# Performance work log

Hardware: AMD Instinct MI355X
Metric: run time of the kernel (lower is better)

Reference implementation:

```python
import jax, jax.numpy as jnp
import numpy as np

B, T, D, U, P, E = 32, 10, 10, 50, 50, 256
EPS_ATTN = 1e-8
EPS_LN = 1e-5


def _layer_norm(x, w, b):
    mu = jnp.mean(x, axis=-1, keepdims=True)
    var = jnp.mean((x - mu) ** 2, axis=-1, keepdims=True)
    return (x - mu) / jnp.sqrt(var + EPS_LN) * w + b


def setup_inputs() -> dict:
    key = jax.random.key(0)
    ks = jax.random.split(key, 8)
    xavier = float(np.sqrt(2.0 / (E + E)))
    return {
        "Q": jax.random.normal(ks[0], (B, T, U, E), dtype=jnp.float32),
        "K": jax.random.normal(ks[1], (B, D, P, E), dtype=jnp.float32),
        "V": jax.random.normal(ks[2], (B, D, P, E), dtype=jnp.float32),
        "attention_mask": jnp.zeros((B, T, D, U, P), dtype=jnp.float32),
        "W1": jax.random.normal(ks[3], (E, E), dtype=jnp.float32) * xavier,
        "b1": jnp.zeros((E,), dtype=jnp.float32),
        "W2": jax.random.normal(ks[4], (E, E), dtype=jnp.float32) * xavier,
        "b2": jnp.zeros((E,), dtype=jnp.float32),
        "ln1_w": jnp.ones((E,), dtype=jnp.float32),
        "ln1_b": jnp.zeros((E,), dtype=jnp.float32),
        "ln2_w": jnp.ones((E,), dtype=jnp.float32),
        "ln2_b": jnp.zeros((E,), dtype=jnp.float32),
    }


def reference(Q, K, V, attention_mask, W1, b1, W2, b2, ln1_w, ln1_b, ln2_w, ln2_b):
    # dk = max(1.0, emb_dim); scale = sqrt(dk) + eps
    scale = jnp.sqrt(jnp.asarray(float(max(1.0, Q.shape[-1])), dtype=Q.dtype)) + EPS_ATTN
    # (B,T,D,U,P) attention logits
    qk = jnp.einsum("btue,bdpe->btdup", Q, K) / scale + attention_mask
    score = jax.nn.softmax(qk, axis=-1)
    v_att = jnp.einsum("btdup,bdpe->btdue", score, V)  # (B,T,D,U,E)
    x = Q[:, :, None, :, :] + v_att  # broadcast over doc dim
    x = _layer_norm(x, ln1_w, ln1_b)
    ffn = jnp.maximum(x @ W1.T + b1, 0.0) @ W2.T + b2
    return _layer_norm(ffn + x, ln2_w, ln2_b)
```

## Files before the change

### kernel.cpp

```cpp
#include <hip/hip_runtime.h>
#include <math.h>

#define Bsz 32
#define Tt  10
#define Dd  10
#define Uu  50
#define Pp  50
#define Ee  256

typedef __attribute__((ext_vector_type(8))) short bf16x8;
typedef __attribute__((ext_vector_type(4))) float f32x4;

#define STK 264
#define STV 72
#define STS 72

#define OFF_A 0
#define OFF_B 33792
#define OFF_C 70656
#define OFF_R 79872
#define SMEM_TOT 80896

__device__ __forceinline__ unsigned short f2bf(float f) {
    unsigned u = __builtin_bit_cast(unsigned, f);
    u += 0x7fffu + ((u >> 16) & 1u);
    return (unsigned short)(u >> 16);
}
__device__ __forceinline__ float bf2f(unsigned short h) {
    unsigned u = ((unsigned)h) << 16;
    return __builtin_bit_cast(float, u);
}
__device__ __forceinline__ bf16x8 ldfrag(const unsigned short* p, int stride, int r0, int c0, int lane) {
    return *(const bf16x8*)(p + (size_t)(r0 + (lane & 15)) * stride + c0 + ((lane >> 4) << 3));
}
__device__ __forceinline__ bf16x8 wfrag(const unsigned short* wbf, const float* wf, int use_ws,
                                        int n, int k0, int lane) {
    const int row = n + (lane & 15);
    const int col = k0 + ((lane >> 4) << 3);
    if (use_ws) {
        return *(const bf16x8*)(wbf + (size_t)row * 256 + col);
    }
    const float4 a = *(const float4*)(wf + (size_t)row * 256 + col);
    const float4 b = *(const float4*)(wf + (size_t)row * 256 + col + 4);
    bf16x8 r;
    r[0] = (short)f2bf(a.x); r[1] = (short)f2bf(a.y); r[2] = (short)f2bf(a.z); r[3] = (short)f2bf(a.w);
    r[4] = (short)f2bf(b.x); r[5] = (short)f2bf(b.y); r[6] = (short)f2bf(b.z); r[7] = (short)f2bf(b.w);
    return r;
}

__global__ void convert_w_kernel(const float* __restrict__ W1, const float* __restrict__ W2,
                                 unsigned short* __restrict__ ws) {
    int i4 = (blockIdx.x * 256 + threadIdx.x) * 4;
    float4 a = *(const float4*)(W1 + i4);
    ushort4 oa; oa.x = f2bf(a.x); oa.y = f2bf(a.y); oa.z = f2bf(a.z); oa.w = f2bf(a.w);
    *(ushort4*)(ws + i4) = oa;
    float4 b = *(const float4*)(W2 + i4);
    ushort4 ob; ob.x = f2bf(b.x); ob.y = f2bf(b.y); ob.z = f2bf(b.z); ob.w = f2bf(b.w);
    *(ushort4*)(ws + 65536 + i4) = ob;
}

__global__ __launch_bounds__(512, 4) void fusion_kernel(
    const float* __restrict__ Q,  const float* __restrict__ K,
    const float* __restrict__ V,  const float* __restrict__ Msk,
    const float* __restrict__ W1, const float* __restrict__ b1,
    const float* __restrict__ W2, const float* __restrict__ b2,
    const float* __restrict__ ln1w, const float* __restrict__ ln1b,
    const float* __restrict__ ln2w, const float* __restrict__ ln2b,
    const unsigned short* __restrict__ wsbf, int use_ws,
    float* __restrict__ out)
{
    __shared__ __align__(16) unsigned char smem[SMEM_TOT];
    unsigned short* sK   = (unsigned short*)(smem + OFF_A);
    unsigned short* sXbf = (unsigned short*)(smem + OFF_A);
    unsigned short* sVt  = (unsigned short*)(smem + OFF_B);
    unsigned short* sH   = (unsigned short*)(smem + OFF_B);
    unsigned short* sS   = (unsigned short*)(smem + OFF_C);
    float*          red2 = (float*)(smem + OFF_C);
    float*          red  = (float*)(smem + OFF_R);

    const int tid  = threadIdx.x;
    const int lane = tid & 63;
    const int wave = tid >> 6;
    const int quad = lane >> 4;
    const int l15  = lane & 15;

    const int btd = blockIdx.x;
    const int b   = btd / (Tt * Dd);
    const int rem = btd % (Tt * Dd);
    const int t   = rem / Dd;
    const int d   = rem % Dd;

    const float* Qb = Q + ((size_t)(b * Tt + t) * Uu) * Ee;
    const float* Kb = K + ((size_t)(b * Dd + d) * Pp) * Ee;
    const float* Vb = V + ((size_t)(b * Dd + d) * Pp) * Ee;
    const float* Mb = Msk + ((size_t)((b * Tt + t) * Dd + d) * Uu) * Pp;
    float*       Ob = out + ((size_t)((b * Tt + t) * Dd + d) * Uu) * Ee;

    for (int i = tid; i < 3200; i += 512) {
        int r = i >> 6, c4 = (i & 63) << 2;
        float4 k = *(const float4*)(Kb + r * Ee + c4);
        ushort4 ok; ok.x = f2bf(k.x); ok.y = f2bf(k.y); ok.z = f2bf(k.z); ok.w = f2bf(k.w);
        *(ushort4*)(sK + r * STK + c4) = ok;
    }
    for (int i = tid; i < 924; i += 512) {
        int r = 50 + i / 66, c = (i % 66) << 2;
        ushort4 z = {0, 0, 0, 0};
        *(ushort4*)(sK + r * STK + c) = z;
    }
    __syncthreads();

    if (wave < 4) {
        const int mt = wave;
        int arow = mt * 16 + l15; if (arow > 49) arow = 49;
        const float* qrow = Qb + (size_t)arow * Ee + (quad << 3);
        f32x4 acc[4];
        #pragma unroll
        for (int i = 0; i < 4; ++i) acc[i] = (f32x4){0.f, 0.f, 0.f, 0.f};
        #pragma unroll
        for (int k0 = 0; k0 < 256; k0 += 32) {
            float4 qa = *(const float4*)(qrow + k0);
            float4 qb = *(const float4*)(qrow + k0 + 4);
            bf16x8 a;
            a[0] = (short)f2bf(qa.x); a[1] = (short)f2bf(qa.y); a[2] = (short)f2bf(qa.z); a[3] = (short)f2bf(qa.w);
            a[4] = (short)f2bf(qb.x); a[5] = (short)f2bf(qb.y); a[6] = (short)f2bf(qb.z); a[7] = (short)f2bf(qb.w);
            #pragma unroll
            for (int nt = 0; nt < 4; ++nt) {
                bf16x8 bf = ldfrag(sK, STK, nt << 4, k0, lane);
                acc[nt] = __builtin_amdgcn_mfma_f32_16x16x32_bf16(a, bf, acc[nt], 0, 0, 0);
            }
        }
        float l[4][4];
        #pragma unroll
        for (int nt = 0; nt < 4; ++nt) {
            int p = (nt << 4) + l15;
            #pragma unroll
            for (int r = 0; r < 4; ++r) {
                int u = mt * 16 + (quad << 2) + r;
                float v = acc[nt][r] * 0.0625f;
                if (p < Pp) { if (u < Uu) v += Mb[u * Pp + p]; }
                else v = -1e30f;
                l[nt][r] = v;
            }
        }
        #pragma unroll
        for (int r = 0; r < 4; ++r) {
            float m = fmaxf(fmaxf(l[0][r], l[1][r]), fmaxf(l[2][r], l[3][r]));
            #pragma unroll
            for (int msk = 1; msk < 16; msk <<= 1) m = fmaxf(m, __shfl_xor(m, msk));
            float e0 = __expf(l[0][r] - m), e1 = __expf(l[1][r] - m);
            float e2 = __expf(l[2][r] - m), e3 = __expf(l[3][r] - m);
            float s = e0 + e1 + e2 + e3;
            #pragma unroll
            for (int msk = 1; msk < 16; msk <<= 1) s += __shfl_xor(s, msk);
            float inv = 1.0f / s;
            int u = mt * 16 + (quad << 2) + r;
            sS[u * STS +  0 + l15] = f2bf(e0 * inv);
            sS[u * STS + 16 + l15] = f2bf(e1 * inv);
            sS[u * STS + 32 + l15] = f2bf(e2 * inv);
            sS[u * STS + 48 + l15] = f2bf(e3 * inv);
        }
    } else {
        const int lt = tid - 256;
        #pragma unroll 4
        for (int i = lt; i < 12800; i += 256) {
            int p = i >> 8, e = i & 255;
            sVt[e * STV + p] = f2bf(Vb[p * Ee + e]);
        }
        for (int i = lt; i < 3584; i += 256) {
            int p = 50 + (i >> 8), e = i & 255;
            sVt[e * STV + p] = 0;
        }
    }
    __syncthreads();

    {
        const int mt = wave >> 1;
        const int nh = (wave & 1) << 7;
        f32x4 acc[8];
        #pragma unroll
        for (int i = 0; i < 8; ++i) acc[i] = (f32x4){0.f, 0.f, 0.f, 0.f};
        #pragma unroll
        for (int k0 = 0; k0 < 64; k0 += 32) {
            bf16x8 a = ldfrag(sS, STS, mt << 4, k0, lane);
            #pragma unroll
            for (int nt = 0; nt < 8; ++nt) {
                bf16x8 bf = ldfrag(sVt, STV, nh + (nt << 4), k0, lane);
                acc[nt] = __builtin_amdgcn_mfma_f32_16x16x32_bf16(a, bf, acc[nt], 0, 0, 0);
            }
        }
        float s1[4] = {0.f, 0.f, 0.f, 0.f}, s2[4] = {0.f, 0.f, 0.f, 0.f};
        #pragma unroll
        for (int nt = 0; nt < 8; ++nt) {
            int e = nh + (nt << 4) + l15;
            #pragma unroll
            for (int r = 0; r < 4; ++r) {
                int u = (mt << 4) + (quad << 2) + r;
                float x = 0.f;
                if (u < Uu) x = acc[nt][r] + Qb[(size_t)u * Ee + e];
                acc[nt][r] = x;
                s1[r] += x; s2[r] += x * x;
            }
        }
        #pragma unroll
        for (int msk = 1; msk < 16; msk <<= 1) {
            #pragma unroll
            for (int r = 0; r < 4; ++r) { s1[r] += __shfl_xor(s1[r], msk); s2[r] += __shfl_xor(s2[r], msk); }
        }
        if (l15 == 0) {
            #pragma unroll
            for (int r = 0; r < 4; ++r) {
                int u = (mt << 4) + (quad << 2) + r;
                red[u * 4 + (wave & 1) * 2 + 0] = s1[r];
                red[u * 4 + (wave & 1) * 2 + 1] = s2[r];
            }
        }
        __syncthreads();
        float mu[4], rstd[4];
        #pragma unroll
        for (int r = 0; r < 4; ++r) {
            int u = (mt << 4) + (quad << 2) + r;
            float sum = red[u * 4 + 0] + red[u * 4 + 2];
            float sq  = red[u * 4 + 1] + red[u * 4 + 3];
            mu[r] = sum * (1.0f / 256.0f);
            float var = sq * (1.0f / 256.0f) - mu[r] * mu[r];
            rstd[r] = rsqrtf(var + 1e-5f);
        }
        __syncthreads();
        #pragma unroll
        for (int nt = 0; nt < 8; ++nt) {
            int e = nh + (nt << 4) + l15;
            float wv = ln1w[e], bv = ln1b[e];
            #pragma unroll
            for (int r = 0; r < 4; ++r) {
                int u = (mt << 4) + (quad << 2) + r;
                float o = (u < Uu) ? ((acc[nt][r] - mu[r]) * rstd[r] * wv + bv) : 0.f;
                sXbf[u * STK + e] = f2bf(o);
            }
        }
    }
    __syncthreads();

    const int mp = wave >> 2;
    const int nq = wave & 3;
    {
        f32x4 acc2[2][4];
        #pragma unroll
        for (int mi = 0; mi < 2; ++mi)
            #pragma unroll
            for (int nt = 0; nt < 4; ++nt) acc2[mi][nt] = (f32x4){0.f, 0.f, 0.f, 0.f};
        float b1v[4];
        #pragma unroll
        for (int nt = 0; nt < 4; ++nt) b1v[nt] = b1[(nq << 6) + (nt << 4) + l15];
        #pragma unroll
        for (int k0 = 0; k0 < 256; k0 += 32) {
            bf16x8 a0 = ldfrag(sXbf, STK, (mp << 5),      k0, lane);
            bf16x8 a1 = ldfrag(sXbf, STK, (mp << 5) + 16, k0, lane);
            #pragma unroll
            for (int nt = 0; nt < 4; ++nt) {
                bf16x8 bf = wfrag(wsbf, W1, use_ws, (nq << 6) + (nt << 4), k0, lane);
                acc2[0][nt] = __builtin_amdgcn_mfma_f32_16x16x32_bf16(a0, bf, acc2[0][nt], 0, 0, 0);
                acc2[1][nt] = __builtin_amdgcn_mfma_f32_16x16x32_bf16(a1, bf, acc2[1][nt], 0, 0, 0);
            }
        }
        #pragma unroll
        for (int mi = 0; mi < 2; ++mi)
            #pragma unroll
            for (int nt = 0; nt < 4; ++nt) {
                int j = (nq << 6) + (nt << 4) + l15;
                #pragma unroll
                for (int r = 0; r < 4; ++r) {
                    int u = (mp << 5) + (mi << 4) + (quad << 2) + r;
                    sH[u * STK + j] = f2bf(fmaxf(acc2[mi][nt][r] + b1v[nt], 0.f));
                }
            }
    }
    __syncthreads();

    {
        f32x4 acc2[2][4];
        #pragma unroll
        for (int mi = 0; mi < 2; ++mi)
            #pragma unroll
            for (int nt = 0; nt < 4; ++nt) acc2[mi][nt] = (f32x4){0.f, 0.f, 0.f, 0.f};
        float b2v[4], w2l[4], b2l[4];
        #pragma unroll
        for (int nt = 0; nt < 4; ++nt) {
            int j = (nq << 6) + (nt << 4) + l15;
            b2v[nt] = b2[j]; w2l[nt] = ln2w[j]; b2l[nt] = ln2b[j];
        }
        #pragma unroll
        for (int k0 = 0; k0 < 256; k0 += 32) {
            bf16x8 a0 = ldfrag(sH, STK, (mp << 5),      k0, lane);
            bf16x8 a1 = ldfrag(sH, STK, (mp << 5) + 16, k0, lane);
            #pragma unroll
            for (int nt = 0; nt < 4; ++nt) {
                bf16x8 bf = wfrag(wsbf + 65536, W2, use_ws, (nq << 6) + (nt << 4), k0, lane);
                acc2[0][nt] = __builtin_amdgcn_mfma_f32_16x16x32_bf16(a0, bf, acc2[0][nt], 0, 0, 0);
                acc2[1][nt] = __builtin_amdgcn_mfma_f32_16x16x32_bf16(a1, bf, acc2[1][nt], 0, 0, 0);
            }
        }
        float s1[2][4], s2[2][4];
        #pragma unroll
        for (int mi = 0; mi < 2; ++mi)
            #pragma unroll
            for (int r = 0; r < 4; ++r) { s1[mi][r] = 0.f; s2[mi][r] = 0.f; }
        #pragma unroll
        for (int mi = 0; mi < 2; ++mi)
            #pragma unroll
            for (int nt = 0; nt < 4; ++nt) {
                int j = (nq << 6) + (nt << 4) + l15;
                #pragma unroll
                for (int r = 0; r < 4; ++r) {
                    int u = (mp << 5) + (mi << 4) + (quad << 2) + r;
                    float y = acc2[mi][nt][r] + b2v[nt] + bf2f(sXbf[u * STK + j]);
                    acc2[mi][nt][r] = y;
                    s1[mi][r] += y; s2[mi][r] += y * y;
                }
            }
        #pragma unroll
        for (int msk = 1; msk < 16; msk <<= 1)
            #pragma unroll
            for (int mi = 0; mi < 2; ++mi)
                #pragma unroll
                for (int r = 0; r < 4; ++r) {
                    s1[mi][r] += __shfl_xor(s1[mi][r], msk);
                    s2[mi][r] += __shfl_xor(s2[mi][r], msk);
                }
        if (l15 == 0) {
            #pragma unroll
            for (int mi = 0; mi < 2; ++mi)
                #pragma unroll
                for (int r = 0; r < 4; ++r) {
                    int u = (mp << 5) + (mi << 4) + (quad << 2) + r;
                    red2[u * 8 + nq * 2 + 0] = s1[mi][r];
                    red2[u * 8 + nq * 2 + 1] = s2[mi][r];
                }
        }
        __syncthreads();
        #pragma unroll
        for (int mi = 0; mi < 2; ++mi)
            #pragma unroll
            for (int r = 0; r < 4; ++r) {
                int u = (mp << 5) + (mi << 4) + (quad << 2) + r;
                if (u < Uu) {
                    float sum = red2[u * 8 + 0] + red2[u * 8 + 2] + red2[u * 8 + 4] + red2[u * 8 + 6];
                    float sq  = red2[u * 8 + 1] + red2[u * 8 + 3] + red2[u * 8 + 5] + red2[u * 8 + 7];
                    float mu = sum * (1.0f / 256.0f);
                    float var = sq * (1.0f / 256.0f) - mu * mu;
                    float rstd = rsqrtf(var + 1e-5f);
                    #pragma unroll
                    for (int nt = 0; nt < 4; ++nt) {
                        int j = (nq << 6) + (nt << 4) + l15;
                        Ob[(size_t)u * Ee + j] = (acc2[mi][nt][r] - mu) * rstd * w2l[nt] + b2l[nt];
                    }
                }
            }
    }
}

extern "C" void kernel_launch(void* const* d_in, const int* in_sizes, int n_in,
                              void* d_out, int out_size, void* d_ws, size_t ws_size,
                              hipStream_t stream) {
    const float* Q    = (const float*)d_in[0];
    const float* K    = (const float*)d_in[1];
    const float* V    = (const float*)d_in[2];
    const float* M    = (const float*)d_in[3];
    const float* W1   = (const float*)d_in[4];
    const float* b1   = (const float*)d_in[5];
    const float* W2   = (const float*)d_in[6];
    const float* b2   = (const float*)d_in[7];
    const float* ln1w = (const float*)d_in[8];
    const float* ln1b = (const float*)d_in[9];
    const float* ln2w = (const float*)d_in[10];
    const float* ln2b = (const float*)d_in[11];
    float* out = (float*)d_out;

    int use_ws = (ws_size >= 262144) ? 1 : 0;
    const unsigned short* wsbf = (const unsigned short*)d_ws;
    if (use_ws) {
        convert_w_kernel<<<64, 256, 0, stream>>>(W1, W2, (unsigned short*)d_ws);
    }
    fusion_kernel<<<Bsz * Tt * Dd, 512, 0, stream>>>(Q, K, V, M, W1, b1, W2, b2,
                                                     ln1w, ln1b, ln2w, ln2b,
                                                     wsbf, use_ws, out);
}
```

Measured before the change: 600.5 us.

## Alias shared-memory buffers to cut LDS footprint and raise block occupancy

Shared memory is compacted by aliasing the K, V-transpose, LN1 output and FFN hidden buffers onto one region. The V transpose load now runs after the QK/softmax stage across all 512 threads, where before it overlapped with softmax on half the block. The residual values are held in packed registers before sH overwrites sXbf. LDS drops from about 80KB to 48KB and launch bounds rise to 6 blocks per CU. Block indices are also swizzled across batches. In exchange the kernel loses the overlap of the V load with the softmax stage, adds a barrier, and raises register pressure.

```diff
diff --git a/kernel.cpp b/kernel.cpp
--- a/kernel.cpp
+++ b/kernel.cpp
@@ -16,10 +16,9 @@
 #define STS 72
 
 #define OFF_A 0
-#define OFF_B 33792
-#define OFF_C 70656
-#define OFF_R 79872
-#define SMEM_TOT 80896
+#define OFF_B 36864
+#define OFF_C 46080
+#define SMEM_TOT 48128
 
 __device__ __forceinline__ unsigned short f2bf(float f) {
     unsigned u = __builtin_bit_cast(unsigned, f);
@@ -59,7 +58,7 @@
     *(ushort4*)(ws + 65536 + i4) = ob;
 }
 
-__global__ __launch_bounds__(512, 4) void fusion_kernel(
+__global__ __launch_bounds__(512, 6) void fusion_kernel(
     const float* __restrict__ Q,  const float* __restrict__ K,
     const float* __restrict__ V,  const float* __restrict__ Msk,
     const float* __restrict__ W1, const float* __restrict__ b1,
@@ -71,12 +70,12 @@
 {
     __shared__ __align__(16) unsigned char smem[SMEM_TOT];
     unsigned short* sK   = (unsigned short*)(smem + OFF_A);
+    unsigned short* sVt  = (unsigned short*)(smem + OFF_A);
     unsigned short* sXbf = (unsigned short*)(smem + OFF_A);
-    unsigned short* sVt  = (unsigned short*)(smem + OFF_B);
-    unsigned short* sH   = (unsigned short*)(smem + OFF_B);
-    unsigned short* sS   = (unsigned short*)(smem + OFF_C);
+    unsigned short* sH   = (unsigned short*)(smem + OFF_A);
+    unsigned short* sS   = (unsigned short*)(smem + OFF_B);
+    float*          red  = (float*)(smem + OFF_C);
     float*          red2 = (float*)(smem + OFF_C);
-    float*          red  = (float*)(smem + OFF_R);
 
     const int tid  = threadIdx.x;
     const int lane = tid & 63;
@@ -84,7 +83,7 @@
     const int quad = lane >> 4;
     const int l15  = lane & 15;
 
-    const int btd = blockIdx.x;
+    const int btd = ((blockIdx.x & 7) * 400) + (blockIdx.x >> 3);
     const int b   = btd / (Tt * Dd);
     const int rem = btd % (Tt * Dd);
     const int t   = rem / Dd;
@@ -159,17 +158,16 @@
             sS[u * STS + 32 + l15] = f2bf(e2 * inv);
             sS[u * STS + 48 + l15] = f2bf(e3 * inv);
         }
-    } else {
-        const int lt = tid - 256;
-        #pragma unroll 4
-        for (int i = lt; i < 12800; i += 256) {
-            int p = i >> 8, e = i & 255;
-            sVt[e * STV + p] = f2bf(Vb[p * Ee + e]);
-        }
-        for (int i = lt; i < 3584; i += 256) {
-            int p = 50 + (i >> 8), e = i & 255;
-            sVt[e * STV + p] = 0;
-        }
+    }
+    __syncthreads();
+
+    for (int i = tid; i < 12800; i += 512) {
+        int p = i >> 8, e = i & 255;
+        sVt[e * STV + p] = f2bf(Vb[p * Ee + e]);
+    }
+    for (int i = tid; i < 3584; i += 512) {
+        int p = 50 + (i >> 8), e = i & 255;
+        sVt[e * STV + p] = 0;
     }
     __syncthreads();
 
@@ -225,7 +223,6 @@
             float var = sq * (1.0f / 256.0f) - mu[r] * mu[r];
             rstd[r] = rsqrtf(var + 1e-5f);
         }
-        __syncthreads();
         #pragma unroll
         for (int nt = 0; nt < 8; ++nt) {
             int e = nh + (nt << 4) + l15;
@@ -242,6 +239,7 @@
 
     const int mp = wave >> 2;
     const int nq = wave & 3;
+    unsigned resid[2][4][2];
     {
         f32x4 acc2[2][4];
         #pragma unroll
@@ -268,6 +266,20 @@
             for (int nt = 0; nt < 4; ++nt) {
                 int j = (nq << 6) + (nt << 4) + l15;
                 #pragma unroll
+                for (int rp = 0; rp < 2; ++rp) {
+                    int u0 = (mp << 5) + (mi << 4) + (quad << 2) + rp * 2;
+                    unsigned lo = sXbf[(size_t)u0 * STK + j];
+                    unsigned hi = sXbf[(size_t)(u0 + 1) * STK + j];
+                    resid[mi][nt][rp] = lo | (hi << 16);
+                }
+            }
+        __syncthreads();
+        #pragma unroll
+        for (int mi = 0; mi < 2; ++mi)
+            #pragma unroll
+            for (int nt = 0; nt < 4; ++nt) {
+                int j = (nq << 6) + (nt << 4) + l15;
+                #pragma unroll
                 for (int r = 0; r < 4; ++r) {
                     int u = (mp << 5) + (mi << 4) + (quad << 2) + r;
                     sH[u * STK + j] = f2bf(fmaxf(acc2[mi][nt][r] + b1v[nt], 0.f));
@@ -308,11 +320,11 @@
         for (int mi = 0; mi < 2; ++mi)
             #pragma unroll
             for (int nt = 0; nt < 4; ++nt) {
-                int j = (nq << 6) + (nt << 4) + l15;
                 #pragma unroll
                 for (int r = 0; r < 4; ++r) {
-                    int u = (mp << 5) + (mi << 4) + (quad << 2) + r;
-                    float y = acc2[mi][nt][r] + b2v[nt] + bf2f(sXbf[u * STK + j]);
+                    unsigned pk = resid[mi][nt][r >> 1];
+                    unsigned short rb = (r & 1) ? (unsigned short)(pk >> 16) : (unsigned short)(pk & 0xffffu);
+                    float y = acc2[mi][nt][r] + b2v[nt] + bf2f(rb);
                     acc2[mi][nt][r] = y;
                     s1[mi][r] += y; s2[mi][r] += y * y;
                 }
```

Result: no change. 608.7 us (+1.4%).
